# Kernel tuning notes

Hardware: AMD Instinct MI355X
Metric: run time of the kernel (lower is better)

## Reference

```python
import jax, jax.numpy as jnp
import numpy as np

N_HEADS = 16


def setup_inputs() -> dict:
    key = jax.random.key(0)
    ks = jax.random.split(key, 5)
    E = 1024
    x = jax.random.normal(ks[0], (2, 2048, E), dtype=jnp.float32)
    s = 1.0 / np.sqrt(E)
    Wq = jax.random.normal(ks[1], (E, E), dtype=jnp.float32) * s
    Wk = jax.random.normal(ks[2], (E, E), dtype=jnp.float32) * s
    Wv = jax.random.normal(ks[3], (E, E), dtype=jnp.float32) * s
    Wo = jax.random.normal(ks[4], (E, E), dtype=jnp.float32) * s
    bo = jnp.zeros((E,), dtype=jnp.float32)
    return {"x": x, "Wq": Wq, "Wk": Wk, "Wv": Wv, "Wo": Wo, "bo": bo}


def reference(x, Wq, Wk, Wv, Wo, bo):
    B, S, E = x.shape
    H = N_HEADS
    D = E // H
    # project and split heads: [B, H, S, D]
    def split_heads(y):
        return y.reshape(B, S, H, D).transpose(0, 2, 1, 3)
    q = split_heads(x @ Wq)
    k = split_heads(x @ Wk)
    v = split_heads(x @ Wv)
    # full score matrix [B, H, S, S]
    scores = jnp.einsum('bhqd,bhkd->bhqk', q, k)
    causal = jnp.triu(jnp.ones((S, S), dtype=bool), k=1)
    scores = jnp.where(causal, -jnp.inf, scores)
    attn = jax.nn.softmax(scores / jnp.sqrt(jnp.float32(D)), axis=-1)
    # dropout rate is 0.0 -> identity
    ctx = jnp.einsum('bhqk,bhkd->bhqd', attn, v)
    ctx = ctx.transpose(0, 2, 1, 3).reshape(B, S, E)
    return ctx @ Wo + bo
```

## Files before the change

### kernel.cpp

```cpp
#include <hip/hip_runtime.h>
#include <stdint.h>


#define N_HEADS 16
#define HD 64
#define SEQ 2048
#define EMB 1024

typedef __attribute__((ext_vector_type(8))) short s16x8;
typedef __attribute__((ext_vector_type(4))) float f32x4;
typedef __attribute__((ext_vector_type(16))) float f32x16;

#define QSCALE 0.18033688f

template <bool B> struct BC { static constexpr bool value = B; };

__device__ __forceinline__ short f2b(float f) {
  union { float f; uint32_t u; } v; v.f = f;
  uint32_t u = v.u;
  u += 0x7fffu + ((u >> 16) & 1u);
  return (short)(u >> 16);
}

__device__ __forceinline__ uint32_t pk2(float a, float b) {
  union { float f; uint32_t u; } x, y; x.f = a; y.f = b;
  return ((x.u + 0x8000u) >> 16) | ((y.u + 0x8000u) & 0xffff0000u);
}

__device__ __forceinline__ float exp2a(float x) {
  float r; asm("v_exp_f32 %0, %1" : "=v"(r) : "v"(x)); return r;
}

__device__ __forceinline__ void gll16(const void* g, void* l) {
  __builtin_amdgcn_global_load_lds((const __attribute__((address_space(1))) void*)g,
                                   (__attribute__((address_space(3))) void*)l, 16, 0, 0);
}

#define SWZ(row, chunk) ((((row) * 8) + ((chunk) ^ ((row) & 7))) * 8)

__global__ __launch_bounds__(256) void k_prep(const float* __restrict__ x,
                                              const float* __restrict__ W0,
                                              const float* __restrict__ W1,
                                              const float* __restrict__ W2,
                                              const float* __restrict__ W3,
                                              short* __restrict__ xb,
                                              short* __restrict__ wt) {
  const int z = blockIdx.x, t = threadIdx.x;
  if (z < 4096) {
    int i = z * 256 + t;
    float4 v = ((const float4*)x)[i];
    short4 o;
    o.x = f2b(v.x); o.y = f2b(v.y); o.z = f2b(v.z); o.w = f2b(v.w);
    ((short4*)xb)[i] = o;
  } else {
    __shared__ float tile[32][33];
    int bz = z - 4096;
    int w = bz >> 10, rem = bz & 1023;
    int bn = (rem & 31) * 32, bk = (rem >> 5) * 32;
    const float* W = w == 0 ? W0 : w == 1 ? W1 : w == 2 ? W2 : W3;
    short* o = wt + (size_t)w * EMB * EMB;
    int tx = t & 31, ty = t >> 5;
    for (int i = ty; i < 32; i += 8)
      tile[i][tx] = W[(size_t)(bk + i) * EMB + bn + tx];
    __syncthreads();
    for (int i = ty; i < 32; i += 8)
      o[(size_t)(bn + i) * EMB + bk + tx] = f2b(tile[tx][i]);
  }
}

__global__ __launch_bounds__(512, 2) void k_qkv(const short* __restrict__ A,
                                                const short* __restrict__ BT,
                                                short* __restrict__ qkv) {
  __shared__ alignas(16) short smem[65536];
  const int t = threadIdx.x;
  const int bx = blockIdx.x, by = blockIdx.y;
  const int m0 = bx * 256;
  const short* Bp = BT + (size_t)by * (256 * EMB);
  const int wave = t >> 6, lane = t & 63;
  const int ml = lane & 15, quad = lane >> 4;
  const int wm = (wave >> 2) * 128, wn = (wave & 3) * 64;
  const int wsel = by >> 2;

  auto stage = [&](int kt) {
    short* sa = smem + (kt & 3) * 16384;
    short* sb = sa + 8192;
    const int k0 = kt * 32;
#pragma unroll
    for (int j = 0; j < 2; j++) {
      int ci = j * 512 + t;
      int r = ci >> 2;
      int col = ((ci & 3) ^ (r & 3)) * 8;
      size_t ldso = (size_t)(j * 512 + (t & ~63)) * 8;
      gll16(A + (size_t)(m0 + r) * EMB + k0 + col, sa + ldso);
      gll16(Bp + (size_t)r * EMB + k0 + col, sb + ldso);
    }
  };

  f32x4 acc[8][4] = {};

  stage(0); stage(1); stage(2);

  auto kloop = [&](auto SWC) {
    constexpr bool SW = decltype(SWC)::value;
    for (int T = 0; T < 32; T++) {
      const short* sa = smem + (T & 3) * 16384;
      const short* sb = sa + 8192;
      if (T < 30) asm volatile("s_waitcnt vmcnt(8)" ::: "memory");
      else        asm volatile("s_waitcnt vmcnt(0)" ::: "memory");
      __builtin_amdgcn_s_barrier();
      __builtin_amdgcn_sched_barrier(0);
      if (T + 3 < 32) stage(T + 3);
      s16x8 af[8];
#pragma unroll
      for (int mt = 0; mt < 8; mt++) {
        int row = wm + mt * 16 + ml;
        af[mt] = *(const s16x8*)&sa[row * 32 + ((quad ^ (row & 3)) * 8)];
      }
#pragma unroll
      for (int n2 = 0; n2 < 2; n2++) {
        int r0 = wn + (n2 * 2 + 0) * 16 + ml;
        int r1 = wn + (n2 * 2 + 1) * 16 + ml;
        s16x8 b0 = *(const s16x8*)&sb[r0 * 32 + ((quad ^ (r0 & 3)) * 8)];
        s16x8 b1 = *(const s16x8*)&sb[r1 * 32 + ((quad ^ (r1 & 3)) * 8)];
        __builtin_amdgcn_s_setprio(1);
#pragma unroll
        for (int mt = 0; mt < 8; mt++) {
          if (SW) {
            acc[mt][n2 * 2 + 0] = __builtin_amdgcn_mfma_f32_16x16x32_bf16(b0, af[mt], acc[mt][n2 * 2 + 0], 0, 0, 0);
            acc[mt][n2 * 2 + 1] = __builtin_amdgcn_mfma_f32_16x16x32_bf16(b1, af[mt], acc[mt][n2 * 2 + 1], 0, 0, 0);
          } else {
            acc[mt][n2 * 2 + 0] = __builtin_amdgcn_mfma_f32_16x16x32_bf16(af[mt], b0, acc[mt][n2 * 2 + 0], 0, 0, 0);
            acc[mt][n2 * 2 + 1] = __builtin_amdgcn_mfma_f32_16x16x32_bf16(af[mt], b1, acc[mt][n2 * 2 + 1], 0, 0, 0);
          }
        }
        __builtin_amdgcn_s_setprio(0);
      }
    }
  };

  if (wsel < 2) kloop(BC<true>{});
  else          kloop(BC<false>{});

  __syncthreads();

  const int b = m0 >> 11, s0 = m0 & (SEQ - 1);
  const int n0in = (by & 3) * 256;
  if (wsel < 2) {
    short* ob = qkv + (size_t)wsel * (4u * 1024 * 1024);
    const float qs = (wsel == 0) ? QSCALE : 1.0f;
#pragma unroll
    for (int half = 0; half < 2; half++) {
      if ((wm >> 7) == half) {
#pragma unroll
        for (int mt = 0; mt < 8; mt++) {
          int lr = mt * 16 + ml;
#pragma unroll
          for (int nt = 0; nt < 4; nt++) {
            uint2 w;
            w.x = pk2(acc[mt][nt][0] * qs, acc[mt][nt][1] * qs);
            w.y = pk2(acc[mt][nt][2] * qs, acc[mt][nt][3] * qs);
            *(uint2*)&smem[lr * 264 + wn + nt * 16 + quad * 4] = w;
          }
        }
      }
      __syncthreads();
#pragma unroll
      for (int p = 0; p < 8; p++) {
        int r = p * 16 + (t >> 5), c = t & 31;
        int e = n0in + c * 8, hh = e >> 6, dd = e & 63;
        *(uint4*)&ob[(((size_t)(b * N_HEADS + hh) * SEQ) + s0 + half * 128 + r) * 64 + dd] =
            *(const uint4*)&smem[r * 264 + c * 8];
      }
      __syncthreads();
    }
  } else {
    short* obv = qkv + (size_t)8 * 1024 * 1024;
#pragma unroll
    for (int half = 0; half < 2; half++) {
      if ((wm >> 7) == half) {
#pragma unroll
        for (int mt = 0; mt < 8; mt++) {
          int lr = mt * 16 + quad * 4;
#pragma unroll
          for (int nt = 0; nt < 4; nt++) {
            int colL = wn + nt * 16 + ml;
            uint2 w;
            w.x = pk2(acc[mt][nt][0], acc[mt][nt][1]);
            w.y = pk2(acc[mt][nt][2], acc[mt][nt][3]);
            *(uint2*)&smem[colL * 136 + lr] = w;
          }
        }
      }
      __syncthreads();
#pragma unroll
      for (int p = 0; p < 8; p++) {
        int colL = p * 32 + (t >> 4);
        int sc = (t & 15) * 8;
        int e = n0in + colL, hh = e >> 6, dd = e & 63;
        *(uint4*)&obv[((size_t)(b * N_HEADS + hh) * HD + dd) * SEQ + s0 + half * 128 + sc] =
            *(const uint4*)&smem[colL * 136 + sc];
      }
      __syncthreads();
    }
  }
}

template <int MODE>
__global__ __launch_bounds__(256) void k_gemm(const short* __restrict__ A,
                                              const short* __restrict__ BT,
                                              void* __restrict__ outp,
                                              const float* __restrict__ bias) {
  __shared__ alignas(16) short smem[4 * 4096];

  const int t = threadIdx.x;
  const int by = blockIdx.y;
  const int m0 = blockIdx.x * 128;
  const short* Bp = BT + (size_t)by * (128 * EMB);
  const int wave = t >> 6, lane = t & 63;
  const int wm = (wave >> 1) * 64, wn = (wave & 1) * 64;
  const int l31 = lane & 31, lh = lane >> 5;

  const int srow = lane >> 2;
  const int soff = ((lane & 3) ^ (srow & 3)) * 8;

  auto stage = [&](int kb, int p) {
    short* as = smem + p * 4096;
    short* bs = smem + 8192 + p * 4096;
#pragma unroll
    for (int i = 0; i < 2; i++) {
      int rb = wave * 32 + i * 16;
      gll16(A + (size_t)(m0 + rb + srow) * EMB + kb + soff, &as[rb * 32]);
      gll16(Bp + (size_t)(rb + srow) * EMB + kb + soff, &bs[rb * 32]);
    }
  };
  auto frd = [&](const short* sb, int row, int kh) -> s16x8 {
    int c = kh * 2 + lh;
    return *(const s16x8*)&sb[row * 32 + ((c ^ (row & 3)) * 8)];
  };

  f32x16 acc[2][2] = {};

  {
    int pb = 0;
    stage(0, 0);
    for (int kb = 0; kb < EMB; kb += 32) {
      __syncthreads();
      if (kb + 32 < EMB) stage(kb + 32, pb ^ 1);
      const short* as = smem + pb * 4096;
      const short* bs = smem + 8192 + pb * 4096;
      s16x8 af[2][2], bf[2][2];
#pragma unroll
      for (int mt = 0; mt < 2; mt++)
#pragma unroll
        for (int kh = 0; kh < 2; kh++) af[mt][kh] = frd(as, wm + mt * 32 + l31, kh);
#pragma unroll
      for (int nt = 0; nt < 2; nt++)
#pragma unroll
        for (int kh = 0; kh < 2; kh++) bf[nt][kh] = frd(bs, wn + nt * 32 + l31, kh);
#pragma unroll
      for (int mt = 0; mt < 2; mt++)
#pragma unroll
        for (int nt = 0; nt < 2; nt++)
#pragma unroll
          for (int kh = 0; kh < 2; kh++)
            acc[mt][nt] = __builtin_amdgcn_mfma_f32_32x32x16_bf16(bf[nt][kh], af[mt][kh], acc[mt][nt], 0, 0, 0);
      pb ^= 1;
    }
  }

  {
    float* of = (float*)outp;
    const int n0 = by * 128;
#pragma unroll
    for (int mt = 0; mt < 2; mt++) {
      int mg = m0 + wm + mt * 32 + l31;
#pragma unroll
      for (int nt = 0; nt < 2; nt++)
#pragma unroll
        for (int g = 0; g < 4; g++) {
          int ng = n0 + wn + nt * 32 + g * 8 + 4 * lh;
          f32x4 bv = *(const f32x4*)&bias[ng];
          f32x4 w;
          w[0] = acc[mt][nt][4 * g + 0] + bv[0];
          w[1] = acc[mt][nt][4 * g + 1] + bv[1];
          w[2] = acc[mt][nt][4 * g + 2] + bv[2];
          w[3] = acc[mt][nt][4 * g + 3] + bv[3];
          *(f32x4*)&of[(size_t)mg * EMB + ng] = w;
        }
    }
  }
}

__global__ __launch_bounds__(512) void k_attn(const short* __restrict__ Q,
                                              const short* __restrict__ K,
                                              const short* __restrict__ Vt,
                                              short* __restrict__ ctx) {
  __shared__ alignas(16) short UQP[128 * 72];
  __shared__ alignas(16) short Ks0[64 * 64], Ks1[64 * 64];
  __shared__ alignas(16) short Vs0[64 * 64], Vs1[64 * 64];

  const int t = threadIdx.x, wave = t >> 6, lane = t & 63;
  const int ml = lane & 15, quad = lane >> 4;
  const int bh = blockIdx.x;
  const int qb = 15 - (int)blockIdx.y;
  const size_t base = (size_t)bh * SEQ * HD;
  const int q0 = qb * 128, wq = q0 + wave * 16;

  const int sr = lane >> 3;
  const int sc = ((lane & 7) ^ sr) * 8;

#pragma unroll
  for (int i = 0; i < 2; i++) {
    int r8 = wave * 16 + i * 8;
    gll16(Q + base + (size_t)(q0 + r8 + sr) * HD + sc, &UQP[r8 * 64]);
  }
  auto stageKV = [&](int kt, short* kd, short* vd) {
    const int kbase = kt * 64;
    const int r8 = wave * 8;
    gll16(K + base + (size_t)(kbase + r8 + sr) * HD + sc, &kd[r8 * 64]);
    gll16(Vt + base + (size_t)(r8 + sr) * SEQ + kbase + sc, &vd[r8 * 64]);
  };

  f32x4 cacc[4] = {};
  float li = 0.f;
  short* Pw = &UQP[wave * 16 * 72];

  stageKV(0, Ks0, Vs0);
  __syncthreads();

  s16x8 qf[2];
#pragma unroll
  for (int c = 0; c < 2; c++)
    qf[c] = *(const s16x8*)&UQP[SWZ(wave * 16 + ml, 4 * c + quad)];
  __syncthreads();

  auto tile_body = [&](int kt, const short* kd, const short* vd) {
    const int kbase = kt * 64;
    if (kbase > wq + 15) return;
    const bool diag = (kbase + 63 > wq);
    f32x4 st[4];
#pragma unroll
    for (int nt = 0; nt < 4; nt++) {
      int row = nt * 16 + ml;
      s16x8 kf0 = *(const s16x8*)&kd[SWZ(row, quad)];
      s16x8 kf1 = *(const s16x8*)&kd[SWZ(row, 4 + quad)];
      f32x4 z = {};
      z = __builtin_amdgcn_mfma_f32_16x16x32_bf16(kf0, qf[0], z, 0, 0, 0);
      st[nt] = __builtin_amdgcn_mfma_f32_16x16x32_bf16(kf1, qf[1], z, 0, 0, 0);
    }
    const int qg = wq + ml;
    float rsum = 0.f;
#pragma unroll
    for (int nt = 0; nt < 4; nt++) {
      float p0 = exp2a(st[nt][0]);
      float p1 = exp2a(st[nt][1]);
      float p2 = exp2a(st[nt][2]);
      float p3 = exp2a(st[nt][3]);
      if (diag) {
        int kk = kbase + nt * 16 + quad * 4;
        if (kk + 0 > qg) p0 = 0.f;
        if (kk + 1 > qg) p1 = 0.f;
        if (kk + 2 > qg) p2 = 0.f;
        if (kk + 3 > qg) p3 = 0.f;
      }
      rsum += (p0 + p1) + (p2 + p3);
      uint2 w; w.x = pk2(p0, p1); w.y = pk2(p2, p3);
      *(uint2*)&Pw[ml * 72 + nt * 16 + quad * 4] = w;
    }
    li += rsum;
    __builtin_amdgcn_wave_barrier();

    s16x8 pf[2];
#pragma unroll
    for (int c = 0; c < 2; c++)
      pf[c] = *(const s16x8*)&Pw[ml * 72 + c * 32 + quad * 8];
#pragma unroll
    for (int mt = 0; mt < 4; mt++) {
      int row = mt * 16 + ml;
      s16x8 vf0 = *(const s16x8*)&vd[SWZ(row, quad)];
      s16x8 vf1 = *(const s16x8*)&vd[SWZ(row, 4 + quad)];
      cacc[mt] = __builtin_amdgcn_mfma_f32_16x16x32_bf16(vf0, pf[0], cacc[mt], 0, 0, 0);
      cacc[mt] = __builtin_amdgcn_mfma_f32_16x16x32_bf16(vf1, pf[1], cacc[mt], 0, 0, 0);
    }
  };

  const int nkt = 2 * qb + 2;
  for (int kt = 0; kt < nkt; kt += 2) {
    stageKV(kt + 1, Ks1, Vs1);
    tile_body(kt, Ks0, Vs0);
    __syncthreads();
    if (kt + 2 < nkt) stageKV(kt + 2, Ks0, Vs0);
    tile_body(kt + 1, Ks1, Vs1);
    __syncthreads();
  }

  li += __shfl_xor(li, 16, 64);
  li += __shfl_xor(li, 32, 64);
  float inv = 1.0f / li;
#pragma unroll
  for (int mt = 0; mt < 4; mt++) {
    uint2 w;
    w.x = pk2(cacc[mt][0] * inv, cacc[mt][1] * inv);
    w.y = pk2(cacc[mt][2] * inv, cacc[mt][3] * inv);
    *(uint2*)&Pw[ml * 72 + mt * 16 + quad * 4] = w;
  }
  __builtin_amdgcn_wave_barrier();
  const int b = bh >> 4, h = bh & 15;
#pragma unroll
  for (int i = 0; i < 2; i++) {
    int row = i * 8 + (lane >> 3);
    int q = wq + row;
    size_t gbase = ((size_t)(b * SEQ + q)) * EMB + h * 64 + (lane & 7) * 8;
    *(uint4*)&ctx[gbase] = *(const uint4*)&Pw[row * 72 + (lane & 7) * 8];
  }
}

extern "C" void kernel_launch(void* const* d_in, const int* in_sizes, int n_in,
                              void* d_out, int out_size, void* d_ws, size_t ws_size,
                              hipStream_t stream) {
  const float* x  = (const float*)d_in[0];
  const float* Wq = (const float*)d_in[1];
  const float* Wk = (const float*)d_in[2];
  const float* Wv = (const float*)d_in[3];
  const float* Wo = (const float*)d_in[4];
  const float* bo = (const float*)d_in[5];
  float* out = (float*)d_out;

  short* ws = (short*)d_ws;
  short* xb  = ws;
  short* wt  = ws + (size_t)4 * 1024 * 1024;
  short* qkv = ws + (size_t)8 * 1024 * 1024;

  k_prep<<<8192, 256, 0, stream>>>(x, Wq, Wk, Wv, Wo, xb, wt);
  k_qkv<<<dim3(16, 12), 512, 0, stream>>>(xb, wt, qkv);
  k_attn<<<dim3(32, 16), 512, 0, stream>>>(qkv, qkv + (size_t)4 * 1024 * 1024,
                                           qkv + (size_t)8 * 1024 * 1024, xb);
  k_gemm<1><<<dim3(32, 8), 256, 0, stream>>>(xb, wt + (size_t)3 * 1024 * 1024, out, bo);
}
```

Before: 174.1 us.

## Give each attention wave 32 query rows with 4 waves per block

The attention kernel now runs 4 waves of 256 threads per block instead of 8, and each wave handles two 16-row query sub-tiles. Every K and V fragment read from shared memory is therefore reused for two MFMAs, halving LDS fragment traffic per FLOP. Each thread now stages two K/V rows per tile. In exchange, register pressure and per-thread serial work roughly double, and fewer waves per block are available to hide latency. The causal early-exit now works at 32-row granularity, so slightly more masked work is done near the diagonal.

```diff
diff --git a/kernel.cpp b/kernel.cpp
--- a/kernel.cpp
+++ b/kernel.cpp
@@ -291,11 +291,11 @@
   }
 }
 
-__global__ __launch_bounds__(512) void k_attn(const short* __restrict__ Q,
+__global__ __launch_bounds__(256) void k_attn(const short* __restrict__ Q,
                                               const short* __restrict__ K,
                                               const short* __restrict__ Vt,
                                               short* __restrict__ ctx) {
-  __shared__ alignas(16) short UQP[128 * 72];
+  __shared__ alignas(16) short UQP[4 * 2304];
   __shared__ alignas(16) short Ks0[64 * 64], Ks1[64 * 64];
   __shared__ alignas(16) short Vs0[64 * 64], Vs1[64 * 64];
 
@@ -304,83 +304,99 @@
   const int bh = blockIdx.x;
   const int qb = 15 - (int)blockIdx.y;
   const size_t base = (size_t)bh * SEQ * HD;
-  const int q0 = qb * 128, wq = q0 + wave * 16;
+  const int q0 = qb * 128, wq = q0 + wave * 32;
 
   const int sr = lane >> 3;
   const int sc = ((lane & 7) ^ sr) * 8;
 
 #pragma unroll
-  for (int i = 0; i < 2; i++) {
-    int r8 = wave * 16 + i * 8;
+  for (int i = 0; i < 4; i++) {
+    int r8 = wave * 32 + i * 8;
     gll16(Q + base + (size_t)(q0 + r8 + sr) * HD + sc, &UQP[r8 * 64]);
   }
   auto stageKV = [&](int kt, short* kd, short* vd) {
     const int kbase = kt * 64;
-    const int r8 = wave * 8;
-    gll16(K + base + (size_t)(kbase + r8 + sr) * HD + sc, &kd[r8 * 64]);
-    gll16(Vt + base + (size_t)(r8 + sr) * SEQ + kbase + sc, &vd[r8 * 64]);
-  };
-
-  f32x4 cacc[4] = {};
-  float li = 0.f;
-  short* Pw = &UQP[wave * 16 * 72];
+#pragma unroll
+    for (int j = 0; j < 2; j++) {
+      int r8 = wave * 16 + j * 8;
+      gll16(K + base + (size_t)(kbase + r8 + sr) * HD + sc, &kd[r8 * 64]);
+      gll16(Vt + base + (size_t)(r8 + sr) * SEQ + kbase + sc, &vd[r8 * 64]);
+    }
+  };
+
+  f32x4 cacc[4][2] = {};
+  float li[2] = {0.f, 0.f};
+  short* Pw = &UQP[wave * 2304];
 
   stageKV(0, Ks0, Vs0);
   __syncthreads();
 
-  s16x8 qf[2];
-#pragma unroll
-  for (int c = 0; c < 2; c++)
-    qf[c] = *(const s16x8*)&UQP[SWZ(wave * 16 + ml, 4 * c + quad)];
+  s16x8 qf[2][2];
+#pragma unroll
+  for (int qt = 0; qt < 2; qt++)
+#pragma unroll
+    for (int c = 0; c < 2; c++)
+      qf[qt][c] = *(const s16x8*)&UQP[SWZ(wave * 32 + qt * 16 + ml, 4 * c + quad)];
   __syncthreads();
 
   auto tile_body = [&](int kt, const short* kd, const short* vd) {
     const int kbase = kt * 64;
-    if (kbase > wq + 15) return;
+    if (kbase > wq + 31) return;
     const bool diag = (kbase + 63 > wq);
-    f32x4 st[4];
+    f32x4 st[4][2];
 #pragma unroll
     for (int nt = 0; nt < 4; nt++) {
       int row = nt * 16 + ml;
       s16x8 kf0 = *(const s16x8*)&kd[SWZ(row, quad)];
       s16x8 kf1 = *(const s16x8*)&kd[SWZ(row, 4 + quad)];
-      f32x4 z = {};
-      z = __builtin_amdgcn_mfma_f32_16x16x32_bf16(kf0, qf[0], z, 0, 0, 0);
-      st[nt] = __builtin_amdgcn_mfma_f32_16x16x32_bf16(kf1, qf[1], z, 0, 0, 0);
-    }
-    const int qg = wq + ml;
-    float rsum = 0.f;
-#pragma unroll
-    for (int nt = 0; nt < 4; nt++) {
-      float p0 = exp2a(st[nt][0]);
-      float p1 = exp2a(st[nt][1]);
-      float p2 = exp2a(st[nt][2]);
-      float p3 = exp2a(st[nt][3]);
-      if (diag) {
-        int kk = kbase + nt * 16 + quad * 4;
-        if (kk + 0 > qg) p0 = 0.f;
-        if (kk + 1 > qg) p1 = 0.f;
-        if (kk + 2 > qg) p2 = 0.f;
-        if (kk + 3 > qg) p3 = 0.f;
-      }
-      rsum += (p0 + p1) + (p2 + p3);
-      uint2 w; w.x = pk2(p0, p1); w.y = pk2(p2, p3);
-      *(uint2*)&Pw[ml * 72 + nt * 16 + quad * 4] = w;
-    }
-    li += rsum;
+#pragma unroll
+      for (int qt = 0; qt < 2; qt++) {
+        f32x4 z = {};
+        z = __builtin_amdgcn_mfma_f32_16x16x32_bf16(kf0, qf[qt][0], z, 0, 0, 0);
+        st[nt][qt] = __builtin_amdgcn_mfma_f32_16x16x32_bf16(kf1, qf[qt][1], z, 0, 0, 0);
+      }
+    }
+#pragma unroll
+    for (int qt = 0; qt < 2; qt++) {
+      const int qgl = wq + qt * 16 + ml;
+      float rsum = 0.f;
+#pragma unroll
+      for (int nt = 0; nt < 4; nt++) {
+        float p0 = exp2a(st[nt][qt][0]);
+        float p1 = exp2a(st[nt][qt][1]);
+        float p2 = exp2a(st[nt][qt][2]);
+        float p3 = exp2a(st[nt][qt][3]);
+        if (diag) {
+          int kk = kbase + nt * 16 + quad * 4;
+          if (kk + 0 > qgl) p0 = 0.f;
+          if (kk + 1 > qgl) p1 = 0.f;
+          if (kk + 2 > qgl) p2 = 0.f;
+          if (kk + 3 > qgl) p3 = 0.f;
+        }
+        rsum += (p0 + p1) + (p2 + p3);
+        uint2 w; w.x = pk2(p0, p1); w.y = pk2(p2, p3);
+        *(uint2*)&Pw[(qt * 16 + ml) * 72 + nt * 16 + quad * 4] = w;
+      }
+      li[qt] += rsum;
+    }
     __builtin_amdgcn_wave_barrier();
 
-    s16x8 pf[2];
-#pragma unroll
-    for (int c = 0; c < 2; c++)
-      pf[c] = *(const s16x8*)&Pw[ml * 72 + c * 32 + quad * 8];
-#pragma unroll
-    for (int mt = 0; mt < 4; mt++) {
-      int row = mt * 16 + ml;
+    s16x8 pf[2][2];
+#pragma unroll
+    for (int qt = 0; qt < 2; qt++)
+#pragma unroll
+      for (int c = 0; c < 2; c++)
+        pf[qt][c] = *(const s16x8*)&Pw[(qt * 16 + ml) * 72 + c * 32 + quad * 8];
+#pragma unroll
+    for (int dt = 0; dt < 4; dt++) {
+      int row = dt * 16 + ml;
       s16x8 vf0 = *(const s16x8*)&vd[SWZ(row, quad)];
       s16x8 vf1 = *(const s16x8*)&vd[SWZ(row, 4 + quad)];
-      cacc[mt] = __builtin_amdgcn_mfma_f32_16x16x32_bf16(vf0, pf[0], cacc[mt], 0, 0, 0);
-      cacc[mt] = __builtin_amdgcn_mfma_f32_16x16x32_bf16(vf1, pf[1], cacc[mt], 0, 0, 0);
+#pragma unroll
+      for (int qt = 0; qt < 2; qt++) {
+        cacc[dt][qt] = __builtin_amdgcn_mfma_f32_16x16x32_bf16(vf0, pf[qt][0], cacc[dt][qt], 0, 0, 0);
+        cacc[dt][qt] = __builtin_amdgcn_mfma_f32_16x16x32_bf16(vf1, pf[qt][1], cacc[dt][qt], 0, 0, 0);
+      }
     }
   };
 
@@ -394,20 +410,23 @@
     __syncthreads();
   }
 
-  li += __shfl_xor(li, 16, 64);
-  li += __shfl_xor(li, 32, 64);
-  float inv = 1.0f / li;
-#pragma unroll
-  for (int mt = 0; mt < 4; mt++) {
-    uint2 w;
-    w.x = pk2(cacc[mt][0] * inv, cacc[mt][1] * inv);
-    w.y = pk2(cacc[mt][2] * inv, cacc[mt][3] * inv);
-    *(uint2*)&Pw[ml * 72 + mt * 16 + quad * 4] = w;
+  li[0] += __shfl_xor(li[0], 16, 64); li[0] += __shfl_xor(li[0], 32, 64);
+  li[1] += __shfl_xor(li[1], 16, 64); li[1] += __shfl_xor(li[1], 32, 64);
+  float inv0 = 1.0f / li[0], inv1 = 1.0f / li[1];
+#pragma unroll
+  for (int dt = 0; dt < 4; dt++) {
+    uint2 w0, w1;
+    w0.x = pk2(cacc[dt][0][0] * inv0, cacc[dt][0][1] * inv0);
+    w0.y = pk2(cacc[dt][0][2] * inv0, cacc[dt][0][3] * inv0);
+    *(uint2*)&Pw[ml * 72 + dt * 16 + quad * 4] = w0;
+    w1.x = pk2(cacc[dt][1][0] * inv1, cacc[dt][1][1] * inv1);
+    w1.y = pk2(cacc[dt][1][2] * inv1, cacc[dt][1][3] * inv1);
+    *(uint2*)&Pw[(16 + ml) * 72 + dt * 16 + quad * 4] = w1;
   }
   __builtin_amdgcn_wave_barrier();
   const int b = bh >> 4, h = bh & 15;
 #pragma unroll
-  for (int i = 0; i < 2; i++) {
+  for (int i = 0; i < 4; i++) {
     int row = i * 8 + (lane >> 3);
     int q = wq + row;
     size_t gbase = ((size_t)(b * SEQ + q)) * EMB + h * 64 + (lane & 7) * 8;
@@ -433,7 +452,7 @@
 
   k_prep<<<8192, 256, 0, stream>>>(x, Wq, Wk, Wv, Wo, xb, wt);
   k_qkv<<<dim3(16, 12), 512, 0, stream>>>(xb, wt, qkv);
-  k_attn<<<dim3(32, 16), 512, 0, stream>>>(qkv, qkv + (size_t)4 * 1024 * 1024,
+  k_attn<<<dim3(32, 16), 256, 0, stream>>>(qkv, qkv + (size_t)4 * 1024 * 1024,
                                            qkv + (size_t)8 * 1024 * 1024, xb);
   k_gemm<1><<<dim3(32, 8), 256, 0, stream>>>(xb, wt + (size_t)3 * 1024 * 1024, out, bo);
 }
```

After: 184.8 us. 1.06x slower.

## Interleave global-to-LDS staging with MFMA phases in QKV GEMM k-loop

Applied to the files above, without the earlier changes.

Splits each k-iteration of the QKV projection GEMM into two phases. Each phase loads two B fragments, issues half of the next-stage global-to-LDS loads, and runs a barrier plus lgkmcnt wait before its MFMA burst. The aim is to spread memory issue across the compute and keep wavefronts in lockstep so loads and MFMAs overlap better. The cost is two extra workgroup barriers per iteration, which may add stalls.

```diff
diff --git a/kernel.cpp b/kernel.cpp
--- a/kernel.cpp
+++ b/kernel.cpp
@@ -81,20 +81,18 @@
   const int wm = (wave >> 2) * 128, wn = (wave & 3) * 64;
   const int wsel = by >> 2;
 
-  auto stage = [&](int kt) {
+  auto stage2 = [&](int kt, int j) {
     short* sa = smem + (kt & 3) * 16384;
     short* sb = sa + 8192;
     const int k0 = kt * 32;
-#pragma unroll
-    for (int j = 0; j < 2; j++) {
-      int ci = j * 512 + t;
-      int r = ci >> 2;
-      int col = ((ci & 3) ^ (r & 3)) * 8;
-      size_t ldso = (size_t)(j * 512 + (t & ~63)) * 8;
-      gll16(A + (size_t)(m0 + r) * EMB + k0 + col, sa + ldso);
-      gll16(Bp + (size_t)r * EMB + k0 + col, sb + ldso);
-    }
-  };
+    int ci = j * 512 + t;
+    int r = ci >> 2;
+    int col = ((ci & 3) ^ (r & 3)) * 8;
+    size_t ldso = (size_t)(j * 512 + (t & ~63)) * 8;
+    gll16(A + (size_t)(m0 + r) * EMB + k0 + col, sa + ldso);
+    gll16(Bp + (size_t)r * EMB + k0 + col, sb + ldso);
+  };
+  auto stage = [&](int kt) { stage2(kt, 0); stage2(kt, 1); };
 
   f32x4 acc[8][4] = {};
 
@@ -109,32 +107,52 @@
       else        asm volatile("s_waitcnt vmcnt(0)" ::: "memory");
       __builtin_amdgcn_s_barrier();
       __builtin_amdgcn_sched_barrier(0);
-      if (T + 3 < 32) stage(T + 3);
+
       s16x8 af[8];
 #pragma unroll
       for (int mt = 0; mt < 8; mt++) {
         int row = wm + mt * 16 + ml;
         af[mt] = *(const s16x8*)&sa[row * 32 + ((quad ^ (row & 3)) * 8)];
       }
-#pragma unroll
-      for (int n2 = 0; n2 < 2; n2++) {
-        int r0 = wn + (n2 * 2 + 0) * 16 + ml;
-        int r1 = wn + (n2 * 2 + 1) * 16 + ml;
-        s16x8 b0 = *(const s16x8*)&sb[r0 * 32 + ((quad ^ (r0 & 3)) * 8)];
-        s16x8 b1 = *(const s16x8*)&sb[r1 * 32 + ((quad ^ (r1 & 3)) * 8)];
-        __builtin_amdgcn_s_setprio(1);
-#pragma unroll
-        for (int mt = 0; mt < 8; mt++) {
-          if (SW) {
-            acc[mt][n2 * 2 + 0] = __builtin_amdgcn_mfma_f32_16x16x32_bf16(b0, af[mt], acc[mt][n2 * 2 + 0], 0, 0, 0);
-            acc[mt][n2 * 2 + 1] = __builtin_amdgcn_mfma_f32_16x16x32_bf16(b1, af[mt], acc[mt][n2 * 2 + 1], 0, 0, 0);
-          } else {
-            acc[mt][n2 * 2 + 0] = __builtin_amdgcn_mfma_f32_16x16x32_bf16(af[mt], b0, acc[mt][n2 * 2 + 0], 0, 0, 0);
-            acc[mt][n2 * 2 + 1] = __builtin_amdgcn_mfma_f32_16x16x32_bf16(af[mt], b1, acc[mt][n2 * 2 + 1], 0, 0, 0);
-          }
+      int r0 = wn + ml, r1 = wn + 16 + ml;
+      s16x8 b0 = *(const s16x8*)&sb[r0 * 32 + ((quad ^ (r0 & 3)) * 8)];
+      s16x8 b1 = *(const s16x8*)&sb[r1 * 32 + ((quad ^ (r1 & 3)) * 8)];
+      if (T + 3 < 32) stage2(T + 3, 0);
+      __builtin_amdgcn_s_barrier();
+      asm volatile("s_waitcnt lgkmcnt(0)" ::: "memory");
+      __builtin_amdgcn_sched_barrier(0);
+      __builtin_amdgcn_s_setprio(1);
+#pragma unroll
+      for (int mt = 0; mt < 8; mt++) {
+        if (SW) {
+          acc[mt][0] = __builtin_amdgcn_mfma_f32_16x16x32_bf16(b0, af[mt], acc[mt][0], 0, 0, 0);
+          acc[mt][1] = __builtin_amdgcn_mfma_f32_16x16x32_bf16(b1, af[mt], acc[mt][1], 0, 0, 0);
+        } else {
+          acc[mt][0] = __builtin_amdgcn_mfma_f32_16x16x32_bf16(af[mt], b0, acc[mt][0], 0, 0, 0);
+          acc[mt][1] = __builtin_amdgcn_mfma_f32_16x16x32_bf16(af[mt], b1, acc[mt][1], 0, 0, 0);
         }
-        __builtin_amdgcn_s_setprio(0);
-      }
+      }
+      __builtin_amdgcn_s_setprio(0);
+
+      int r2 = wn + 32 + ml, r3 = wn + 48 + ml;
+      s16x8 b2 = *(const s16x8*)&sb[r2 * 32 + ((quad ^ (r2 & 3)) * 8)];
+      s16x8 b3 = *(const s16x8*)&sb[r3 * 32 + ((quad ^ (r3 & 3)) * 8)];
+      if (T + 3 < 32) stage2(T + 3, 1);
+      __builtin_amdgcn_s_barrier();
+      asm volatile("s_waitcnt lgkmcnt(0)" ::: "memory");
+      __builtin_amdgcn_sched_barrier(0);
+      __builtin_amdgcn_s_setprio(1);
+#pragma unroll
+      for (int mt = 0; mt < 8; mt++) {
+        if (SW) {
+          acc[mt][2] = __builtin_amdgcn_mfma_f32_16x16x32_bf16(b2, af[mt], acc[mt][2], 0, 0, 0);
+          acc[mt][3] = __builtin_amdgcn_mfma_f32_16x16x32_bf16(b3, af[mt], acc[mt][3], 0, 0, 0);
+        } else {
+          acc[mt][2] = __builtin_amdgcn_mfma_f32_16x16x32_bf16(af[mt], b2, acc[mt][2], 0, 0, 0);
+          acc[mt][3] = __builtin_amdgcn_mfma_f32_16x16x32_bf16(af[mt], b3, acc[mt][3], 0, 0, 0);
+        }
+      }
+      __builtin_amdgcn_s_setprio(0);
     }
   };
 
```

After: 177.9 us. 1.02x slower.
